# Kernel optimization log

Measured on AMD Instinct MI355X. Metric: run time of the kernel, lower is better.

The kernel has to match this reference:

```python
import jax, jax.numpy as jnp
import numpy as np

V, E, H, DV = 32000, 512, 1024, 512
B, K = 64, 49


def setup_inputs():
    key = jax.random.key(0)
    ks = jax.random.split(key, 16)
    p = lambda i, shape: jax.random.normal(ks[i], shape, dtype=jnp.float32) * 0.02
    return {
        "thought": jax.random.normal(ks[0], (B, H), dtype=jnp.float32),
        "visual_features": jax.random.normal(ks[1], (B, K, DV), dtype=jnp.float32),
        "max_len": 64,
        "embedding": p(2, (V, E)),
        "Wih1": p(3, (4 * H, E)), "Whh1": p(4, (4 * H, H)),
        "bih1": jnp.zeros((4 * H,), jnp.float32), "bhh1": jnp.zeros((4 * H,), jnp.float32),
        "Wih2": p(5, (4 * H, H)), "Whh2": p(6, (4 * H, H)),
        "bih2": jnp.zeros((4 * H,), jnp.float32), "bhh2": jnp.zeros((4 * H,), jnp.float32),
        "Wg1": p(7, (H, H)), "bg1": jnp.zeros((H,), jnp.float32),
        "Wg2": p(8, (1, H)), "bg2": jnp.zeros((1,), jnp.float32),
        "Wo": p(9, (V, H)), "bo": jnp.zeros((V,), jnp.float32),
        "Wv": p(10, (H, DV)), "bv": jnp.zeros((H,), jnp.float32),
        "ln_g": jnp.ones((H,), jnp.float32), "ln_b": jnp.zeros((H,), jnp.float32),
    }


def _lstm_cell(x, h, c, Wih, Whh, bih, bhh):
    # PyTorch LSTM gate order: i, f, g, o
    z = x @ Wih.T + h @ Whh.T + bih + bhh
    i, f, g, o = jnp.split(z, 4, axis=-1)
    c_new = jax.nn.sigmoid(f) * c + jax.nn.sigmoid(i) * jnp.tanh(g)
    h_new = jax.nn.sigmoid(o) * jnp.tanh(c_new)
    return h_new, c_new


def reference(thought, visual_features, max_len, embedding, Wih1, Whh1, bih1, bhh1,
              Wih2, Whh2, bih2, bbh2=None, bih2_dummy=None, **_unused):
    raise RuntimeError('placeholder')


def reference(thought, visual_features, max_len, embedding, Wih1, Whh1, bih1, bhh1,
              Wih2, Whh2, bih2, bhh2, Wg1, bg1, Wg2, bg2, Wo, bo, Wv, bv, ln_g, ln_b):
    Bsz, Hd = thought.shape
    temperature = 0.4  # epoch = 0 -> 0.4 + 0.4*0
    top_p = 0.7        # epoch = 0 -> 0.7 + 0.2*0
    scale = 1.0 / jnp.sqrt(jnp.asarray(Hd, jnp.float32))
    # visual_proj: Linear + LayerNorm (Dropout is identity in eval mode)
    vp = visual_features @ Wv.T + bv
    mu = vp.mean(-1, keepdims=True)
    var = vp.var(-1, keepdims=True)
    vp = (vp - mu) / jnp.sqrt(var + 1e-5) * ln_g + ln_b  # [B,K,H]
    b_idx = jnp.arange(Bsz)
    # carry: (h1,c1,h2,c2, input token, last-3 token history, history validity)
    init = (thought, jnp.zeros_like(thought), thought, jnp.zeros_like(thought),
            jnp.full((Bsz,), 1, jnp.int32),
            jnp.zeros((Bsz, 3), jnp.int32), jnp.zeros((Bsz, 3), jnp.bool_))
    keys = jax.random.split(jax.random.key(42), max_len)

    def step(carry, key):
        h1, c1, h2, c2, inp, hist, histv = carry
        emb = embedding[inp]  # [B,E]
        h1, c1 = _lstm_cell(emb, h1, c1, Wih1, Whh1, bih1, bhh1)
        h2, c2 = _lstm_cell(h1, h2, c2, Wih2, Whh2, bih2, bhh2)
        gate = jax.nn.sigmoid(jnp.tanh(h2 @ Wg1.T + bg1) @ Wg2.T + bg2)  # [B,1]
        out = h2 * gate
        attn = jax.nn.softmax(jnp.einsum('bh,bkh->bk', out, vp) * scale, axis=-1)
        out = out + jnp.einsum('bk,bkh->bh', attn, vp)
        logits = out @ Wo.T + bo  # [B,V]
        # repetition penalty: -2.0 once per UNIQUE token in last-3 history (set semantics via .max)
        pen = jnp.zeros_like(logits).at[b_idx[:, None], hist].max(histv.astype(logits.dtype))
        logits = (logits - 2.0 * pen) / temperature
        # nucleus (top-p) filtering, matching top_k_top_p_filtering with top_k=0
        order = jnp.argsort(-logits, axis=-1)
        sl = jnp.take_along_axis(logits, order, axis=-1)
        cum = jnp.cumsum(jax.nn.softmax(sl, axis=-1), axis=-1)
        rem = cum > top_p
        rem = jnp.concatenate([jnp.zeros_like(rem[:, :1]), rem[:, :-1]], axis=-1)
        mask = jnp.zeros_like(rem).at[b_idx[:, None], order].set(rem)
        logits = jnp.where(mask, -jnp.inf, logits)
        nxt = jax.random.categorical(key, logits).astype(jnp.int32)  # multinomial sample
        hist = jnp.concatenate([hist[:, 1:], nxt[:, None]], axis=1)
        histv = jnp.concatenate([histv[:, 1:], jnp.ones((Bsz, 1), jnp.bool_)], axis=1)
        return (h1, c1, h2, c2, nxt, hist, histv), nxt

    _, toks = jax.lax.scan(step, init, keys)
    return toks.T  # [B, max_len]
```

## Files before the change

### kernel.cpp

```cpp
#include <hip/hip_runtime.h>
#include <hip/hip_bf16.h>
#include <stdint.h>


#define B_   64
#define H_   1024
#define E_   512
#define DV_  512
#define KV_  49
#define V_   32000
#define T_   64

__device__ __forceinline__ uint32_t rotl32(uint32_t x, int r) {
  return (x << r) | (x >> (32 - r));
}
__device__ __forceinline__ void tf2x32(uint32_t k0, uint32_t k1,
                                       uint32_t x0, uint32_t x1,
                                       uint32_t& o0, uint32_t& o1) {
  uint32_t ks0 = k0, ks1 = k1, ks2 = k0 ^ k1 ^ 0x1BD11BDAu;
  x0 += ks0; x1 += ks1;
#define RND_(r) { x0 += x1; x1 = rotl32(x1, r) ^ x0; }
  RND_(13) RND_(15) RND_(26) RND_(6)  x0 += ks1; x1 += ks2 + 1u;
  RND_(17) RND_(29) RND_(16) RND_(24) x0 += ks2; x1 += ks0 + 2u;
  RND_(13) RND_(15) RND_(26) RND_(6)  x0 += ks0; x1 += ks1 + 3u;
  RND_(17) RND_(29) RND_(16) RND_(24) x0 += ks1; x1 += ks2 + 4u;
  RND_(13) RND_(15) RND_(26) RND_(6)  x0 += ks2; x1 += ks0 + 5u;
#undef RND_
  o0 = x0; o1 = x1;
}

__device__ __forceinline__ unsigned key_of(float f) {
  unsigned u = __float_as_uint(f);
  return (u & 0x80000000u) ? ~u : (u | 0x80000000u);
}
__device__ __forceinline__ float sigf(float x) { return 1.0f / (1.0f + expf(-x)); }

__global__ __launch_bounds__(256)
void gemm32(const float* __restrict__ A0, int lda0, const float* __restrict__ W0,
            int ldw0, int K0, float* __restrict__ out0, int ldo0, int nt0,
            const float* __restrict__ A1, int lda1, const float* __restrict__ W1,
            int ldw1, int K1, float* __restrict__ out1, int ldo1) {
  __shared__ __align__(16) float As[64][36];
  __shared__ __align__(16) float Ws[32][36];
  int tid = threadIdx.x;
  int bx = blockIdx.x;
  const float* A; const float* W; float* out;
  int lda, ldw, K, ldo, n0;
  if (bx < nt0) { A = A0; W = W0; out = out0; lda = lda0; ldw = ldw0; K = K0; ldo = ldo0; n0 = bx * 32; }
  else          { A = A1; W = W1; out = out1; lda = lda1; ldw = ldw1; K = K1; ldo = ldo1; n0 = (bx - nt0) * 32; }
  int m0 = blockIdx.y * 64;
  int tc = tid & 15, tr = tid >> 4;
  float acc[4][2] = {};
  for (int kc = 0; kc < K; kc += 32) {
#pragma unroll
    for (int l = tid; l < 768; l += 256) {
      if (l < 512) {
        int r = l >> 3, c4 = l & 7;
        *(float4*)&As[r][c4 * 4] =
            *(const float4*)&A[(long long)(m0 + r) * lda + kc + c4 * 4];
      } else {
        int q = l - 512;
        int r = q >> 3, c4 = q & 7;
        *(float4*)&Ws[r][c4 * 4] =
            *(const float4*)&W[(long long)(n0 + r) * ldw + kc + c4 * 4];
      }
    }
    __syncthreads();
#pragma unroll
    for (int kk4 = 0; kk4 < 8; kk4++) {
      float4 a4[4], w4[2];
#pragma unroll
      for (int i = 0; i < 4; i++) a4[i] = *(const float4*)&As[tr * 4 + i][kk4 * 4];
#pragma unroll
      for (int j = 0; j < 2; j++) w4[j] = *(const float4*)&Ws[tc * 2 + j][kk4 * 4];
#pragma unroll
      for (int i = 0; i < 4; i++)
#pragma unroll
        for (int j = 0; j < 2; j++) {
          acc[i][j] = fmaf(a4[i].x, w4[j].x, acc[i][j]);
          acc[i][j] = fmaf(a4[i].y, w4[j].y, acc[i][j]);
          acc[i][j] = fmaf(a4[i].z, w4[j].z, acc[i][j]);
          acc[i][j] = fmaf(a4[i].w, w4[j].w, acc[i][j]);
        }
    }
    __syncthreads();
  }
#pragma unroll
  for (int i = 0; i < 4; i++)
#pragma unroll
    for (int j = 0; j < 2; j++)
      out[(long long)(m0 + tr * 4 + i) * ldo + n0 + tc * 2 + j] = acc[i][j];
}

__global__ __launch_bounds__(256)
void ln_vp(float* __restrict__ vp, const float* __restrict__ bv,
           const float* __restrict__ g, const float* __restrict__ bt) {
  int row = blockIdx.x, tid = threadIdx.x;
  __shared__ float buf[H_];
  __shared__ float red[256];
  float* p = vp + (long long)row * H_;
  for (int h = tid; h < H_; h += 256) buf[h] = __fadd_rn(p[h], bv[h]);
  __syncthreads();
  float s = 0;
  for (int h = tid; h < H_; h += 256) s += buf[h];
  red[tid] = s; __syncthreads();
  for (int off = 128; off > 0; off >>= 1) { if (tid < off) red[tid] += red[tid + off]; __syncthreads(); }
  float mu = red[0] / (float)H_;
  __syncthreads();
  float vs = 0;
  for (int h = tid; h < H_; h += 256) { float d = buf[h] - mu; vs += d * d; }
  red[tid] = vs; __syncthreads();
  for (int off = 128; off > 0; off >>= 1) { if (tid < off) red[tid] += red[tid + off]; __syncthreads(); }
  float var = red[0] / (float)H_;
  float sq = sqrtf(var + 1e-5f);
  for (int h = tid; h < H_; h += 256) {
    float nrm = __fdiv_rn(__fsub_rn(buf[h], mu), sq);
    p[h] = __fadd_rn(__fmul_rn(nrm, g[h]), bt[h]);
  }
}

__global__ __launch_bounds__(256)
void lstm_cell2(const float* __restrict__ dx, const float* __restrict__ dh,
                const float* __restrict__ bih, const float* __restrict__ bhh,
                float* __restrict__ c,
                float* __restrict__ hA, int ldA, float* __restrict__ hB, int ldB) {
  int idx = blockIdx.x * 256 + threadIdx.x;
  int b = idx >> 10, h = idx & 1023;
  float z[4];
#pragma unroll
  for (int g = 0; g < 4; g++) {
    int j = g * 1024 + h;
    float s = __fadd_rn(dx[b * 4096 + j], dh[b * 4096 + j]);
    s = __fadd_rn(s, bih[j]);
    s = __fadd_rn(s, bhh[j]);
    z[g] = s;
  }
  float fc = __fmul_rn(sigf(z[1]), c[idx]);
  float ig = __fmul_rn(sigf(z[0]), tanhf(z[2]));
  float cn = __fadd_rn(fc, ig);
  float hn = __fmul_rn(sigf(z[3]), tanhf(cn));
  c[idx] = cn;
  hA[(long long)b * ldA + h] = hn;
  hB[(long long)b * ldB + h] = hn;
}

__global__ __launch_bounds__(256)
void gate_attn(const float* __restrict__ dg, const float* __restrict__ bg1,
               const float* __restrict__ Wg2, const float* __restrict__ bg2,
               const float* __restrict__ h2buf, const float* __restrict__ vp,
               float* __restrict__ ctx) {
  int b = blockIdx.x, tid = threadIdx.x;
  __shared__ float t1[H_], outv[H_], attn[64];
  __shared__ float gate_s;
  for (int h = tid; h < H_; h += 256)
    t1[h] = tanhf(__fadd_rn(dg[b * H_ + h], bg1[h]));
  __syncthreads();
  if (tid == 0) {
    float s = 0;
    for (int h = 0; h < H_; h++) s = fmaf(t1[h], Wg2[h], s);
    gate_s = sigf(__fadd_rn(s, bg2[0]));
  }
  __syncthreads();
  float gate = gate_s;
  for (int h = tid; h < H_; h += 256) outv[h] = __fmul_rn(h2buf[b * H_ + h], gate);
  __syncthreads();
  if (tid < KV_) {
    const float* vrow = vp + ((long long)b * KV_ + tid) * H_;
    float a = 0;
    for (int h = 0; h < H_; h++) a = fmaf(outv[h], vrow[h], a);
    attn[tid] = __fmul_rn(a, 0.03125f);
  }
  __syncthreads();
  if (tid == 0) {
    float m = -INFINITY;
    for (int k = 0; k < KV_; k++) m = fmaxf(m, attn[k]);
    float ss = 0;
    for (int k = 0; k < KV_; k++) { attn[k] = expf(attn[k] - m); ss += attn[k]; }
    for (int k = 0; k < KV_; k++) attn[k] = __fdiv_rn(attn[k], ss);
  }
  __syncthreads();
  for (int h = tid; h < H_; h += 256) {
    float acc = 0;
    for (int k = 0; k < KV_; k++) acc = fmaf(attn[k], vp[((long long)b * KV_ + k) * H_ + h], acc);
    ctx[b * H_ + h] = __fadd_rn(outv[h], acc);
  }
}

__global__ __launch_bounds__(256)
void init_state(const float* __restrict__ thought, const float* __restrict__ embedding,
                float* c1, float* c2, float* xcat1, float* xcat2,
                int* hist, int* histv) {
  int i = blockIdx.x * 256 + threadIdx.x;
  if (i < B_ * H_) {
    int b = i >> 10, h = i & 1023;
    c1[i] = 0.f; c2[i] = 0.f;
    float th = thought[i];
    xcat1[b * (E_ + H_) + E_ + h] = th;
    xcat2[b * (2 * H_) + H_ + h] = th;
    if (h < E_) xcat1[b * (E_ + H_) + h] = embedding[E_ + h];
  }
  if (i < B_ * 3) { hist[i] = 0; histv[i] = 0; }
}

__global__ __launch_bounds__(1024)
void sample_kernel(const float* __restrict__ dlog, const float* __restrict__ bo,
                   float* __restrict__ Lbuf, float* __restrict__ Ebuf,
                   int* __restrict__ hist, int* __restrict__ histv,
                   const float* __restrict__ embedding, float* __restrict__ xcat1,
                   int* __restrict__ outTok, int t) {
  int b = blockIdx.x, tid = threadIdx.x;
  __shared__ float redf[1024];
  __shared__ int   redi[1024];
  __shared__ unsigned long long binS[256], suf[256];
  __shared__ unsigned binC[256];
  __shared__ int jstar_s;
  __shared__ unsigned long long carry_s;
  __shared__ unsigned prefix_s;

  int hh0 = hist[b * 3 + 0], hh1 = hist[b * 3 + 1], hh2 = hist[b * 3 + 2];
  int p0 = histv[b * 3 + 0] ? hh0 : -1;
  int p1 = histv[b * 3 + 1] ? hh1 : -1;
  int p2 = histv[b * 3 + 2] ? hh2 : -1;
  const float* pa = dlog + (long long)b * V_;
  float* L = Lbuf + (long long)b * V_;
  float* E = Ebuf + (long long)b * V_;

  float lm = -INFINITY;
  for (int v = tid; v < V_; v += 1024) {
    float raw = __fadd_rn(pa[v], bo[v]);
    if (v == p0 || v == p1 || v == p2) raw = __fsub_rn(raw, 2.0f);
    float l = __fdiv_rn(raw, 0.4f);
    L[v] = l;
    lm = fmaxf(lm, l);
  }
  redf[tid] = lm; __syncthreads();
  for (int off = 512; off > 0; off >>= 1) { if (tid < off) redf[tid] = fmaxf(redf[tid], redf[tid + off]); __syncthreads(); }
  float m = redf[0];
  __syncthreads();

  float ls = 0;
  for (int v = tid; v < V_; v += 1024) { float e = expf(L[v] - m); E[v] = e; ls += e; }
  redf[tid] = ls; __syncthreads();
  for (int off = 512; off > 0; off >>= 1) { if (tid < off) redf[tid] += redf[tid + off]; __syncthreads(); }
  float Z = redf[0];
  __syncthreads();

  const double SC = 17592186044416.0;
  const unsigned long long B0 =
      (unsigned long long)(0.699999988079071044921875 * 17592186044416.0);
  if (tid == 0) { carry_s = 0ull; prefix_s = 0u; }
  __syncthreads();
  for (int pass = 0; pass < 4; pass++) {
    int shift = 24 - 8 * pass;
    unsigned maskk = (pass == 0) ? 0u : (0xFFFFFFFFu << (shift + 8));
    if (tid < 256) { binS[tid] = 0ull; binC[tid] = 0u; }
    __syncthreads();
    unsigned pref = prefix_s;
    unsigned long long carry = carry_s;
    for (int v = tid; v < V_; v += 1024) {
      unsigned key = key_of(L[v]);
      if ((key & maskk) == pref) {
        unsigned bin = (key >> shift) & 255u;
        unsigned long long S = (unsigned long long)((double)(E[v] / Z) * SC);
        atomicAdd(&binS[bin], S);
        atomicAdd(&binC[bin], 1u);
      }
    }
    __syncthreads();
    if (tid < 256) suf[tid] = binS[tid];
    __syncthreads();
    for (int off = 1; off < 256; off <<= 1) {
      unsigned long long add = 0ull;
      if (tid < 256 && tid + off < 256) add = suf[tid + off];
      __syncthreads();
      if (tid < 256) suf[tid] += add;
      __syncthreads();
    }
    if (tid == 0) jstar_s = 256;
    __syncthreads();
    if (tid < 256 && binC[tid] > 0u) {
      unsigned long long A = carry + ((tid < 255) ? suf[tid + 1] : 0ull);
      if (A <= B0) atomicMin(&jstar_s, tid);
    }
    __syncthreads();
    if (tid == 0) {
      int j = jstar_s;
      carry_s = carry + ((j < 255) ? suf[j + 1] : 0ull);
      prefix_s = pref | (((unsigned)j) << shift);
    }
    __syncthreads();
  }
  unsigned Kstar = prefix_s;

  unsigned kt0, kt1;
  tf2x32(0u, 42u, 0u, (unsigned)t, kt0, kt1);

  float bestv = -INFINITY; int besti = 0x7fffffff;
  for (int v = tid; v < V_; v += 1024) {
    float l = L[v];
    if (key_of(l) >= Kstar) {
      unsigned r0, r1;
      tf2x32(kt0, kt1, 0u, (unsigned)(b * V_ + v), r0, r1);
      unsigned bits = r0 ^ r1;
      float u = __uint_as_float((bits >> 9) | 0x3f800000u) - 1.0f;
      u = fmaxf(u, 1.17549435e-38f);
      float gum = -logf(-logf(u));
      float val = __fadd_rn(l, gum);
      if (val > bestv) { bestv = val; besti = v; }
    }
  }
  redf[tid] = bestv; redi[tid] = besti; __syncthreads();
  for (int off = 512; off > 0; off >>= 1) {
    if (tid < off) {
      float ov = redf[tid + off]; int oi = redi[tid + off];
      if (ov > redf[tid] || (ov == redf[tid] && oi < redi[tid])) { redf[tid] = ov; redi[tid] = oi; }
    }
    __syncthreads();
  }
  int tok = redi[0];
  if (tid == 0) {
    outTok[b * T_ + t] = tok;
    hist[b * 3 + 0] = hh1; hist[b * 3 + 1] = hh2; hist[b * 3 + 2] = tok;
    int v1 = histv[b * 3 + 1], v2 = histv[b * 3 + 2];
    histv[b * 3 + 0] = v1; histv[b * 3 + 1] = v2; histv[b * 3 + 2] = 1;
  }
  for (int k = tid; k < E_; k += 1024)
    xcat1[b * (E_ + H_) + k] = embedding[(long long)tok * E_ + k];
}

extern "C" void kernel_launch(void* const* d_in, const int* in_sizes, int n_in,
                              void* d_out, int out_size, void* d_ws, size_t ws_size,
                              hipStream_t stream) {
  const float* thought   = (const float*)d_in[0];
  const float* visf      = (const float*)d_in[1];
  const float* embedding = (const float*)d_in[3];
  const float* Wih1 = (const float*)d_in[4];
  const float* Whh1 = (const float*)d_in[5];
  const float* bih1 = (const float*)d_in[6];
  const float* bhh1 = (const float*)d_in[7];
  const float* Wih2 = (const float*)d_in[8];
  const float* Whh2 = (const float*)d_in[9];
  const float* bih2 = (const float*)d_in[10];
  const float* bhh2 = (const float*)d_in[11];
  const float* Wg1  = (const float*)d_in[12];
  const float* bg1  = (const float*)d_in[13];
  const float* Wg2  = (const float*)d_in[14];
  const float* bg2  = (const float*)d_in[15];
  const float* Wo   = (const float*)d_in[16];
  const float* bo   = (const float*)d_in[17];
  const float* Wv   = (const float*)d_in[18];
  const float* bv   = (const float*)d_in[19];
  const float* ln_g = (const float*)d_in[20];
  const float* ln_b = (const float*)d_in[21];
  int* outTok = (int*)d_out;

  float* ws = (float*)d_ws;
  long long off = 0;
  float* vp    = ws + off; off += (long long)B_ * KV_ * H_;
  float* xcat1 = ws + off; off += B_ * (E_ + H_);
  float* xcat2 = ws + off; off += B_ * (2 * H_);
  float* c1    = ws + off; off += B_ * H_;
  float* c2    = ws + off; off += B_ * H_;
  float* h2buf = ws + off; off += B_ * H_;
  float* ctx   = ws + off; off += B_ * H_;
  float* dx    = ws + off; off += (long long)B_ * 4096;
  float* dh    = ws + off; off += (long long)B_ * 4096;
  float* dg    = ws + off; off += (long long)B_ * H_;
  float* dlog  = ws + off; off += (long long)B_ * V_;
  float* Lbuf  = ws + off; off += (long long)B_ * V_;
  float* Ebuf  = ws + off; off += (long long)B_ * V_;
  int* hist  = (int*)(ws + off); off += 256;
  int* histv = (int*)(ws + off); off += 256;

  init_state<<<256, 256, 0, stream>>>(thought, embedding, c1, c2, xcat1, xcat2, hist, histv);

  gemm32<<<dim3(32, KV_), 256, 0, stream>>>(
      visf, DV_, Wv, DV_, DV_, vp, H_, 32,
      visf, DV_, Wv, DV_, DV_, vp, H_);
  ln_vp<<<B_ * KV_, 256, 0, stream>>>(vp, bv, ln_g, ln_b);

  for (int t = 0; t < T_; t++) {
    gemm32<<<dim3(256, 1), 256, 0, stream>>>(
        xcat1, E_ + H_, Wih1, E_, E_, dx, 4096, 128,
        xcat1 + E_, E_ + H_, Whh1, H_, H_, dh, 4096);
    lstm_cell2<<<256, 256, 0, stream>>>(dx, dh, bih1, bhh1, c1,
                                        xcat1 + E_, E_ + H_, xcat2, 2 * H_);
    gemm32<<<dim3(256, 1), 256, 0, stream>>>(
        xcat2, 2 * H_, Wih2, H_, H_, dx, 4096, 128,
        xcat2 + H_, 2 * H_, Whh2, H_, H_, dh, 4096);
    lstm_cell2<<<256, 256, 0, stream>>>(dx, dh, bih2, bhh2, c2,
                                        h2buf, H_, xcat2 + H_, 2 * H_);
    gemm32<<<dim3(32, 1), 256, 0, stream>>>(
        h2buf, H_, Wg1, H_, H_, dg, H_, 32,
        h2buf, H_, Wg1, H_, H_, dg, H_);
    gate_attn<<<B_, 256, 0, stream>>>(dg, bg1, Wg2, bg2, h2buf, vp, ctx);
    gemm32<<<dim3(1000, 1), 256, 0, stream>>>(
        ctx, H_, Wo, H_, H_, dlog, V_, 1000,
        ctx, H_, Wo, H_, H_, dlog, V_);
    sample_kernel<<<B_, 1024, 0, stream>>>(dlog, bo, Lbuf, Ebuf, hist, histv,
                                           embedding, xcat1, outTok, t);
  }
}
```

Measured before the change: 31.85 ms.

## Double-buffer GEMM shared-memory staging with XOR swizzle and templated tile shapes

Replaces the fixed 64x32 GEMM with a templated kernel that prefetches the next K-chunk into registers while computing the current one, using two shared-memory buffers so only one barrier is needed per chunk. Shared-memory rows are XOR-swizzled to cut bank conflicts, and the epilogue writes float4. Tile shapes are tuned per call: 128-wide N tiles with 8x4 per-thread work for the large vocab projection and the visual projection, and 128-thread 4x4 blocks for the LSTM and gate GEMMs. This raises register use and shared memory per block, and gives fewer blocks for the vocab GEMM.

```diff
diff --git a/kernel.cpp b/kernel.cpp
--- a/kernel.cpp
+++ b/kernel.cpp
@@ -35,61 +35,96 @@
 }
 __device__ __forceinline__ float sigf(float x) { return 1.0f / (1.0f + expf(-x)); }
 
-__global__ __launch_bounds__(256)
-void gemm32(const float* __restrict__ A0, int lda0, const float* __restrict__ W0,
-            int ldw0, int K0, float* __restrict__ out0, int ldo0, int nt0,
-            const float* __restrict__ A1, int lda1, const float* __restrict__ W1,
-            int ldw1, int K1, float* __restrict__ out1, int ldo1) {
-  __shared__ __align__(16) float As[64][36];
-  __shared__ __align__(16) float Ws[32][36];
-  int tid = threadIdx.x;
-  int bx = blockIdx.x;
+template <int BN, int TM, int TN, int NTHR>
+__global__ __launch_bounds__(NTHR)
+void gemm_dq(const float* __restrict__ A0, int lda0, const float* __restrict__ W0,
+             int ldw0, int K0, float* __restrict__ out0, int ldo0, int nt0,
+             const float* __restrict__ A1, int lda1, const float* __restrict__ W1,
+             int ldw1, int K1, float* __restrict__ out1, int ldo1) {
+  constexpr int LD = 36;
+  constexpr int ROWS = 64 + BN;
+  constexpr int NF4 = ROWS * 8 / NTHR;
+  constexpr int BUFST = ROWS * LD;
+  constexpr int CG = BN / TN;
+  static_assert(ROWS * 8 % NTHR == 0, "staging divisibility");
+  static_assert((64 / TM) * CG == NTHR, "thread grid");
+  static_assert(TN == 4, "float4 epilogue");
+  __shared__ __align__(16) float S[2][ROWS][LD];
+
+  const int tid = threadIdx.x;
+  const int bx = blockIdx.x;
   const float* A; const float* W; float* out;
   int lda, ldw, K, ldo, n0;
-  if (bx < nt0) { A = A0; W = W0; out = out0; lda = lda0; ldw = ldw0; K = K0; ldo = ldo0; n0 = bx * 32; }
-  else          { A = A1; W = W1; out = out1; lda = lda1; ldw = ldw1; K = K1; ldo = ldo1; n0 = (bx - nt0) * 32; }
-  int m0 = blockIdx.y * 64;
-  int tc = tid & 15, tr = tid >> 4;
-  float acc[4][2] = {};
-  for (int kc = 0; kc < K; kc += 32) {
-#pragma unroll
-    for (int l = tid; l < 768; l += 256) {
-      if (l < 512) {
-        int r = l >> 3, c4 = l & 7;
-        *(float4*)&As[r][c4 * 4] =
-            *(const float4*)&A[(long long)(m0 + r) * lda + kc + c4 * 4];
-      } else {
-        int q = l - 512;
-        int r = q >> 3, c4 = q & 7;
-        *(float4*)&Ws[r][c4 * 4] =
-            *(const float4*)&W[(long long)(n0 + r) * ldw + kc + c4 * 4];
+  if (bx < nt0) { A = A0; W = W0; out = out0; lda = lda0; ldw = ldw0; K = K0; ldo = ldo0; n0 = bx * BN; }
+  else          { A = A1; W = W1; out = out1; lda = lda1; ldw = ldw1; K = K1; ldo = ldo1; n0 = (bx - nt0) * BN; }
+  const int m0 = blockIdx.y * 64;
+  const int tc = tid % CG, tr = tid / CG;
+
+  const float* gp[NF4];
+  float* lp[NF4];
+#pragma unroll
+  for (int q = 0; q < NF4; ++q) {
+    int l = tid + q * NTHR;
+    int r = l >> 3, c4 = l & 7;
+    gp[q] = (l < 512) ? (A + (m0 + r) * lda + c4 * 4)
+                      : (W + (n0 + (r - 64)) * ldw + c4 * 4);
+    lp[q] = &S[0][r][(c4 ^ ((r >> 2) & 7)) << 2];
+  }
+
+  float4 pre[NF4];
+#pragma unroll
+  for (int q = 0; q < NF4; ++q) pre[q] = *(const float4*)gp[q];
+#pragma unroll
+  for (int q = 0; q < NF4; ++q) *(float4*)lp[q] = pre[q];
+  __syncthreads();
+
+  float acc[TM][TN] = {};
+  const int nch = K >> 5;
+  for (int c = 0; c < nch; ++c) {
+    const bool more = (c + 1 < nch);
+    if (more) {
+      const int kc = (c + 1) << 5;
+#pragma unroll
+      for (int q = 0; q < NF4; ++q) pre[q] = *(const float4*)(gp[q] + kc);
+    }
+    const float* Sb = &S[c & 1][0][0];
+#pragma unroll
+    for (int kk = 0; kk < 8; ++kk) {
+      float4 a4[TM], w4[TN];
+#pragma unroll
+      for (int i = 0; i < TM; ++i) {
+        int m = tr * TM + i;
+        a4[i] = *(const float4*)(Sb + m * LD + ((kk ^ ((m >> 2) & 7)) << 2));
       }
-    }
-    __syncthreads();
-#pragma unroll
-    for (int kk4 = 0; kk4 < 8; kk4++) {
-      float4 a4[4], w4[2];
-#pragma unroll
-      for (int i = 0; i < 4; i++) a4[i] = *(const float4*)&As[tr * 4 + i][kk4 * 4];
-#pragma unroll
-      for (int j = 0; j < 2; j++) w4[j] = *(const float4*)&Ws[tc * 2 + j][kk4 * 4];
-#pragma unroll
-      for (int i = 0; i < 4; i++)
-#pragma unroll
-        for (int j = 0; j < 2; j++) {
+#pragma unroll
+      for (int j = 0; j < TN; ++j) {
+        int rw = 64 + tc * TN + j;
+        w4[j] = *(const float4*)(Sb + rw * LD + ((kk ^ ((rw >> 2) & 7)) << 2));
+      }
+#pragma unroll
+      for (int i = 0; i < TM; ++i)
+#pragma unroll
+        for (int j = 0; j < TN; ++j) {
           acc[i][j] = fmaf(a4[i].x, w4[j].x, acc[i][j]);
           acc[i][j] = fmaf(a4[i].y, w4[j].y, acc[i][j]);
           acc[i][j] = fmaf(a4[i].z, w4[j].z, acc[i][j]);
           acc[i][j] = fmaf(a4[i].w, w4[j].w, acc[i][j]);
         }
     }
-    __syncthreads();
-  }
-#pragma unroll
-  for (int i = 0; i < 4; i++)
-#pragma unroll
-    for (int j = 0; j < 2; j++)
-      out[(long long)(m0 + tr * 4 + i) * ldo + n0 + tc * 2 + j] = acc[i][j];
+    if (more) {
+      const int bo = ((c + 1) & 1) * BUFST;
+#pragma unroll
+      for (int q = 0; q < NF4; ++q) *(float4*)(lp[q] + bo) = pre[q];
+    }
+    __syncthreads();
+  }
+
+#pragma unroll
+  for (int i = 0; i < TM; ++i) {
+    float4 o;
+    o.x = acc[i][0]; o.y = acc[i][1]; o.z = acc[i][2]; o.w = acc[i][3];
+    *(float4*)&out[(m0 + tr * TM + i) * ldo + n0 + tc * TN] = o;
+  }
 }
 
 __global__ __launch_bounds__(256)
@@ -374,28 +409,28 @@
 
   init_state<<<256, 256, 0, stream>>>(thought, embedding, c1, c2, xcat1, xcat2, hist, histv);
 
-  gemm32<<<dim3(32, KV_), 256, 0, stream>>>(
-      visf, DV_, Wv, DV_, DV_, vp, H_, 32,
+  gemm_dq<128, 8, 4, 256><<<dim3(8, KV_), 256, 0, stream>>>(
+      visf, DV_, Wv, DV_, DV_, vp, H_, 8,
       visf, DV_, Wv, DV_, DV_, vp, H_);
   ln_vp<<<B_ * KV_, 256, 0, stream>>>(vp, bv, ln_g, ln_b);
 
   for (int t = 0; t < T_; t++) {
-    gemm32<<<dim3(256, 1), 256, 0, stream>>>(
+    gemm_dq<32, 4, 4, 128><<<dim3(256, 1), 128, 0, stream>>>(
         xcat1, E_ + H_, Wih1, E_, E_, dx, 4096, 128,
         xcat1 + E_, E_ + H_, Whh1, H_, H_, dh, 4096);
     lstm_cell2<<<256, 256, 0, stream>>>(dx, dh, bih1, bhh1, c1,
                                         xcat1 + E_, E_ + H_, xcat2, 2 * H_);
-    gemm32<<<dim3(256, 1), 256, 0, stream>>>(
+    gemm_dq<32, 4, 4, 128><<<dim3(256, 1), 128, 0, stream>>>(
         xcat2, 2 * H_, Wih2, H_, H_, dx, 4096, 128,
         xcat2 + H_, 2 * H_, Whh2, H_, H_, dh, 4096);
     lstm_cell2<<<256, 256, 0, stream>>>(dx, dh, bih2, bhh2, c2,
                                         h2buf, H_, xcat2 + H_, 2 * H_);
-    gemm32<<<dim3(32, 1), 256, 0, stream>>>(
+    gemm_dq<32, 4, 4, 128><<<dim3(32, 1), 128, 0, stream>>>(
         h2buf, H_, Wg1, H_, H_, dg, H_, 32,
         h2buf, H_, Wg1, H_, H_, dg, H_);
     gate_attn<<<B_, 256, 0, stream>>>(dg, bg1, Wg2, bg2, h2buf, vp, ctx);
-    gemm32<<<dim3(1000, 1), 256, 0, stream>>>(
-        ctx, H_, Wo, H_, H_, dlog, V_, 1000,
+    gemm_dq<128, 8, 4, 256><<<dim3(250, 1), 256, 0, stream>>>(
+        ctx, H_, Wo, H_, H_, dlog, V_, 250,
         ctx, H_, Wo, H_, H_, dlog, V_);
     sample_kernel<<<B_, 1024, 0, stream>>>(dlog, bo, Lbuf, Ebuf, hist, histv,
                                            embedding, xcat1, outTok, t);
```

After: 31.30 ms. Within noise of the previous version (-1.7%).
